# Kernel optimization log

Measured on AMD Instinct MI355X. Metric: run time of the kernel, lower is better.

Reference implementation:

```python
import jax, jax.numpy as jnp
import numpy as np
import math

B, S, D_IN, D_Q = 4, 2048, 512, 512

def setup_inputs() -> dict:
    key = jax.random.key(0)
    ks = jax.random.split(key, 7)
    s_in = 1.0 / math.sqrt(D_IN)
    x = jax.random.normal(ks[0], (B, S, D_IN), dtype=jnp.float32)
    # nn.Linear-style params: W [out,in], b [out]; uniform(-1/sqrt(in), 1/sqrt(in))
    Wq = jax.random.uniform(ks[1], (D_Q, D_IN), jnp.float32, -s_in, s_in)
    bq = jax.random.uniform(ks[2], (D_Q,), jnp.float32, -s_in, s_in)
    Wk = jax.random.uniform(ks[3], (D_Q, D_IN), jnp.float32, -s_in, s_in)
    bk = jax.random.uniform(ks[4], (D_Q,), jnp.float32, -s_in, s_in)
    Wv = jax.random.uniform(ks[5], (D_Q, D_IN), jnp.float32, -s_in, s_in)
    bv = jax.random.uniform(ks[6], (D_Q,), jnp.float32, -s_in, s_in)
    return {"x": x, "Wq": Wq, "bq": bq, "Wk": Wk, "bk": bk, "Wv": Wv, "bv": bv}

def reference(x, Wq, bq, Wk, bk, Wv, bv):
    # Q/K/V projections: [B,S,D_IN] @ W^T + b -> [B,S,D_Q]
    Q = jnp.einsum('bsi,qi->bsq', x, Wq) + bq
    K = jnp.einsum('bsi,qi->bsq', x, Wk) + bk
    V = jnp.einsum('bsi,qi->bsq', x, Wv) + bv
    scale = 1.0 / math.sqrt(D_Q)
    scores = jnp.einsum('bsq,btq->bst', Q, K) * scale  # [B,S,S]
    attention = jax.nn.softmax(scores, axis=-1)        # 'atten_prob'
    weighted = jnp.einsum('bst,btq->bsq', attention, V)  # 'atten_score'
    return (attention, weighted)
```

## Files before the change

kernel.cpp:

```cpp
#include <hip/hip_runtime.h>
#include <hip/hip_bf16.h>

typedef unsigned short u16;
typedef short bf16x8 __attribute__((ext_vector_type(8)));
typedef float f32x4 __attribute__((ext_vector_type(4)));

#define S_LEN 2048
#define DQ 512
#define NBATCH 4

__device__ __forceinline__ u16 f2bf(float f) {
    __hip_bfloat16 h = __float2bfloat16(f);
    return *reinterpret_cast<u16*>(&h);
}
__device__ __forceinline__ float bf2f(u16 u) {
    unsigned v = ((unsigned)u) << 16;
    union { unsigned u; float f; } c; c.u = v; return c.f;
}

__device__ __forceinline__ void async16(const u16* g, u16* l) {
    __builtin_amdgcn_global_load_lds(
        (__attribute__((address_space(1))) void*)g,
        (__attribute__((address_space(3))) void*)l, 16, 0, 0);
}

__device__ __forceinline__ int xcd_swz(int bid, int chunk) {
    return (bid & 7) * chunk + (bid >> 3);
}

__global__ __launch_bounds__(256) void k_cvt_all(const float* __restrict__ x,
                                                 const float* __restrict__ wq,
                                                 const float* __restrict__ wk,
                                                 const float* __restrict__ wv,
                                                 u16* __restrict__ xb, u16* __restrict__ wb,
                                                 float* __restrict__ sums) {
    int bid = blockIdx.x;
    if (bid >= 4864) {
        int i = (bid - 4864) * 256 + threadIdx.x;
        *(f32x4*)(sums + (size_t)i * 4) = (f32x4)0.0f;
        return;
    }
    const float* src;
    u16* dst;
    int i;
    if (bid < 4096)      { src = x;  dst = xb;          i = bid * 256 + threadIdx.x; }
    else if (bid < 4352) { src = wq; dst = wb;          i = (bid - 4096) * 256 + threadIdx.x; }
    else if (bid < 4608) { src = wk; dst = wb + 262144; i = (bid - 4352) * 256 + threadIdx.x; }
    else                 { src = wv; dst = wb + 524288; i = (bid - 4608) * 256 + threadIdx.x; }
    f32x4 v = *(const f32x4*)(src + (size_t)i * 4);
    ushort4 o;
    o.x = f2bf(v.x); o.y = f2bf(v.y); o.z = f2bf(v.z); o.w = f2bf(v.w);
    *(ushort4*)(dst + (size_t)i * 4) = o;
}

__device__ __forceinline__ void stage_unit(const u16* __restrict__ G, u16* buf,
                                           int kcol, int h, int tid) {
#pragma unroll
    for (int q = 0; q < 2; ++q) {
        int c   = q * 512 + tid;
        int r   = c >> 3;
        int p   = c & 7;
        int lch = p ^ (r & 7);
        async16(G + (size_t)(h * 128 + r) * DQ + kcol + lch * 8,
                buf + h * 8192 + c * 8);
    }
}

__device__ __forceinline__ void gemm256(const u16* __restrict__ A, const u16* __restrict__ B,
                                        u16* ldsA, u16* ldsB, f32x4 acc[8][4], int tid) {
    const int lane = tid & 63;
    const int w    = tid >> 6;
    const int wr   = w >> 2;
    const int wc   = w & 3;
    const int l16  = lane & 15;
    const int quad = lane >> 4;
    const int p0   = quad ^ (l16 & 7);
    const int a0   = (wr * 128 + l16) * 64 + p0 * 8;
    const int a1   = (wr * 128 + l16) * 64 + (p0 ^ 4) * 8;
    const int b0   = (wc * 64 + l16) * 64 + p0 * 8;
    const int b1   = (wc * 64 + l16) * 64 + (p0 ^ 4) * 8;

    stage_unit(A, ldsA, 0, 0, tid);
    stage_unit(A, ldsA, 0, 1, tid);
    stage_unit(B, ldsB, 0, 0, tid);
    stage_unit(B, ldsB, 0, 1, tid);
    __syncthreads();

    for (int kt = 0; kt < 8; ++kt) {
        const u16* rdA = ldsA + (kt & 1) * 16384;
        const u16* rdB = ldsB + (kt & 1) * 16384;
        u16* wrA = ldsA + ((kt + 1) & 1) * 16384;
        u16* wrB = ldsB + ((kt + 1) & 1) * 16384;
        const int  kc = (kt + 1) * 64;
        const bool pf = kt < 7;
        bf16x8 a[4][2], bbf[2][2];

        if (pf) { stage_unit(A, wrA, kc, 0, tid); stage_unit(A, wrA, kc, 1, tid); }
#pragma unroll
        for (int i = 0; i < 4; ++i) {
            a[i][0] = *(const bf16x8*)(rdA + a0 + i * 1024);
            a[i][1] = *(const bf16x8*)(rdA + a1 + i * 1024);
        }
#pragma unroll
        for (int j = 0; j < 2; ++j) {
            bbf[j][0] = *(const bf16x8*)(rdB + b0 + j * 1024);
            bbf[j][1] = *(const bf16x8*)(rdB + b1 + j * 1024);
        }
        __builtin_amdgcn_s_setprio(1);
#pragma unroll
        for (int i = 0; i < 4; ++i)
#pragma unroll
            for (int j = 0; j < 2; ++j) {
                acc[i][j] = __builtin_amdgcn_mfma_f32_16x16x32_bf16(a[i][0], bbf[j][0], acc[i][j], 0, 0, 0);
                acc[i][j] = __builtin_amdgcn_mfma_f32_16x16x32_bf16(a[i][1], bbf[j][1], acc[i][j], 0, 0, 0);
            }
        __builtin_amdgcn_s_setprio(0);

        if (pf) { stage_unit(B, wrB, kc, 0, tid); stage_unit(B, wrB, kc, 1, tid); }
#pragma unroll
        for (int j = 0; j < 2; ++j) {
            bbf[j][0] = *(const bf16x8*)(rdB + b0 + (2 + j) * 1024);
            bbf[j][1] = *(const bf16x8*)(rdB + b1 + (2 + j) * 1024);
        }
        __builtin_amdgcn_s_setprio(1);
#pragma unroll
        for (int i = 0; i < 4; ++i)
#pragma unroll
            for (int j = 0; j < 2; ++j) {
                acc[i][2 + j] = __builtin_amdgcn_mfma_f32_16x16x32_bf16(a[i][0], bbf[j][0], acc[i][2 + j], 0, 0, 0);
                acc[i][2 + j] = __builtin_amdgcn_mfma_f32_16x16x32_bf16(a[i][1], bbf[j][1], acc[i][2 + j], 0, 0, 0);
            }
        __builtin_amdgcn_s_setprio(0);

#pragma unroll
        for (int i = 0; i < 4; ++i) {
            a[i][0] = *(const bf16x8*)(rdA + a0 + (4 + i) * 1024);
            a[i][1] = *(const bf16x8*)(rdA + a1 + (4 + i) * 1024);
        }
        __builtin_amdgcn_s_setprio(1);
#pragma unroll
        for (int i = 0; i < 4; ++i)
#pragma unroll
            for (int j = 0; j < 2; ++j) {
                acc[4 + i][2 + j] = __builtin_amdgcn_mfma_f32_16x16x32_bf16(a[i][0], bbf[j][0], acc[4 + i][2 + j], 0, 0, 0);
                acc[4 + i][2 + j] = __builtin_amdgcn_mfma_f32_16x16x32_bf16(a[i][1], bbf[j][1], acc[4 + i][2 + j], 0, 0, 0);
            }
        __builtin_amdgcn_s_setprio(0);

#pragma unroll
        for (int j = 0; j < 2; ++j) {
            bbf[j][0] = *(const bf16x8*)(rdB + b0 + j * 1024);
            bbf[j][1] = *(const bf16x8*)(rdB + b1 + j * 1024);
        }
        __builtin_amdgcn_s_setprio(1);
#pragma unroll
        for (int i = 0; i < 4; ++i)
#pragma unroll
            for (int j = 0; j < 2; ++j) {
                acc[4 + i][j] = __builtin_amdgcn_mfma_f32_16x16x32_bf16(a[i][0], bbf[j][0], acc[4 + i][j], 0, 0, 0);
                acc[4 + i][j] = __builtin_amdgcn_mfma_f32_16x16x32_bf16(a[i][1], bbf[j][1], acc[4 + i][j], 0, 0, 0);
            }
        __builtin_amdgcn_s_setprio(0);

        __syncthreads();
    }
}

__global__ __launch_bounds__(512, 2) void k_proj(const u16* __restrict__ xb, const u16* __restrict__ Wb,
                                                 const float* __restrict__ bq, const float* __restrict__ bk,
                                                 const float* __restrict__ bv, u16* __restrict__ out,
                                                 u16* __restrict__ VT) {
    __shared__ __align__(16) u16 lds[65536];
    const int l  = xcd_swz(blockIdx.x, 24);
    const int bx = l & 1;
    const int by = (l >> 1) & 31;
    const int z  = l >> 6;
    const int m0 = by * 256, n0 = bx * 256;
    const u16* A = xb + (size_t)m0 * DQ;
    const u16* B = Wb + (size_t)z * DQ * DQ + (size_t)n0 * DQ;
    const float* bias = (z == 0) ? bq : (z == 1) ? bk : bv;

    f32x4 acc[8][4];
#pragma unroll
    for (int i = 0; i < 8; ++i)
#pragma unroll
        for (int j = 0; j < 4; ++j) acc[i][j] = (f32x4)0.0f;

    const int tid = threadIdx.x;
    gemm256(A, B, lds, lds + 32768, acc, tid);

    const int lane = tid & 63, w = tid >> 6;
    const int wr = w >> 2, wc = w & 3;
    const int l16 = lane & 15, quad = lane >> 4;

    if (z < 2) {
        u16* outz = out + (size_t)z * 8192 * DQ;
#pragma unroll
        for (int j = 0; j < 4; ++j) {
            int gn = n0 + wc * 64 + j * 16 + l16;
            float bv_ = bias[gn];
#pragma unroll
            for (int i = 0; i < 8; ++i)
#pragma unroll
                for (int r = 0; r < 4; ++r) {
                    int gm = m0 + wr * 128 + i * 16 + quad * 4 + r;
                    outz[(size_t)gm * DQ + gn] = f2bf(acc[i][j][r] + bv_);
                }
        }
    } else {
        const int bb_ = m0 >> 11;
        u16* VTb_ = VT + (size_t)bb_ * DQ * S_LEN;
#pragma unroll
        for (int j = 0; j < 4; ++j) {
            int gn = n0 + wc * 64 + j * 16 + l16;
            float bv_ = bias[gn];
#pragma unroll
            for (int i = 0; i < 8; ++i) {
                int t0 = (m0 & 2047) + wr * 128 + i * 16 + quad * 4;
                ushort4 o;
                o.x = f2bf(acc[i][j][0] + bv_);
                o.y = f2bf(acc[i][j][1] + bv_);
                o.z = f2bf(acc[i][j][2] + bv_);
                o.w = f2bf(acc[i][j][3] + bv_);
                *(ushort4*)(VTb_ + (size_t)gn * S_LEN + t0) = o;
            }
        }
    }
}

__global__ __launch_bounds__(512, 2) void k_scores(const u16* __restrict__ Qb, const u16* __restrict__ Kb,
                                                   u16* __restrict__ Pb, float* __restrict__ sums) {
    __shared__ __align__(16) u16 lds[65536];
    const int l  = xcd_swz(blockIdx.x, 32);
    const int bx = l & 7;
    const int by = (l >> 3) & 7;
    const int b  = l >> 6;
    const int m0 = by * 256, n0 = bx * 256;
    const u16* A = Qb + ((size_t)b * S_LEN + m0) * DQ;
    const u16* B = Kb + ((size_t)b * S_LEN + n0) * DQ;

    f32x4 acc[8][4];
#pragma unroll
    for (int i = 0; i < 8; ++i)
#pragma unroll
        for (int j = 0; j < 4; ++j) acc[i][j] = (f32x4)0.0f;

    const int tid = threadIdx.x;
    gemm256(A, B, lds, lds + 32768, acc, tid);

    const float scale = 0.044194173824159216f;
    const int lane = tid & 63, w = tid >> 6;
    const int wr = w >> 2, wc = w & 3;
    const int l16 = lane & 15, quad = lane >> 4;
    u16* prow = Pb + (size_t)(b * S_LEN + m0) * S_LEN;

    float psum[8][4];
#pragma unroll
    for (int i = 0; i < 8; ++i)
#pragma unroll
        for (int r = 0; r < 4; ++r) psum[i][r] = 0.0f;

#pragma unroll
    for (int i = 0; i < 8; ++i)
#pragma unroll
        for (int j = 0; j < 4; ++j)
#pragma unroll
            for (int r = 0; r < 4; ++r) {
                int gm = wr * 128 + i * 16 + quad * 4 + r;
                int gn = n0 + wc * 64 + j * 16 + l16;
                float e = __expf(acc[i][j][r] * scale);
                u16 pbv = f2bf(e);
                prow[(size_t)gm * S_LEN + gn] = pbv;
                psum[i][r] += bf2f(pbv);
            }

    float* sums_row = sums + b * S_LEN + m0 + wr * 128;
#pragma unroll
    for (int i = 0; i < 8; ++i)
#pragma unroll
        for (int r = 0; r < 4; ++r) {
            float v = psum[i][r];
            v += __shfl_xor(v, 1);
            v += __shfl_xor(v, 2);
            v += __shfl_xor(v, 4);
            v += __shfl_xor(v, 8);
            if (l16 == 0) atomicAdd(&sums_row[i * 16 + quad * 4 + r], v);
        }
}

__device__ __forceinline__ void stage_pv(const u16* __restrict__ G, u16* buf,
                                         int kcol, int h, int tid) {
    int c   = tid;
    int r   = c >> 3;
    int p   = c & 7;
    int lch = p ^ (r & 7);
    async16(G + (size_t)(h * 64 + r) * S_LEN + kcol + lch * 8,
            buf + h * 4096 + c * 8);
}

__global__ __launch_bounds__(512, 2) void k_pv(const u16* __restrict__ Pb, const u16* __restrict__ VT,
                                               const float* __restrict__ sums,
                                               float* __restrict__ probs,
                                               float* __restrict__ wout) {
    __shared__ __align__(16) u16 lds[49408];
    u16* ldsA = lds;
    u16* ldsB = lds + 24576;
    float* ldsInv = (float*)(lds + 49152);
    const int l  = xcd_swz(blockIdx.x, 32);
    const int bx = l & 3;
    const int by = (l >> 2) & 15;
    const int b  = l >> 6;
    const int m0 = by * 128, n0 = bx * 128;
    const u16* A = Pb + (size_t)(b * S_LEN + m0) * S_LEN;
    const u16* B = VT + (size_t)b * DQ * S_LEN + (size_t)n0 * S_LEN;
    const u16* Psl = Pb + (size_t)(b * S_LEN + m0) * S_LEN + bx * 512;
    float* Pro = probs + ((size_t)b * S_LEN + m0) * S_LEN + bx * 512;

    const int tid  = threadIdx.x;
    const int lane = tid & 63;
    const int w    = tid >> 6;
    const int wr   = w >> 2;
    const int wc   = w & 3;
    const int l16  = lane & 15;
    const int quad = lane >> 4;
    const int p0   = quad ^ (l16 & 7);
    const int a0   = (wr * 64 + l16) * 64 + p0 * 8;
    const int a1   = (wr * 64 + l16) * 64 + (p0 ^ 4) * 8;
    const int b0   = (wc * 32 + l16) * 64 + p0 * 8;
    const int b1   = (wc * 32 + l16) * 64 + (p0 ^ 4) * 8;

    f32x4 acc[4][2];
#pragma unroll
    for (int i = 0; i < 4; ++i)
#pragma unroll
        for (int j = 0; j < 2; ++j) acc[i][j] = (f32x4)0.0f;

    float sv = 1.0f;
    if (tid < 128) sv = sums[b * S_LEN + m0 + tid];
    stage_pv(A, ldsA, 0, 0, tid);          stage_pv(A, ldsA, 0, 1, tid);
    stage_pv(B, ldsB, 0, 0, tid);          stage_pv(B, ldsB, 0, 1, tid);
    stage_pv(A, ldsA + 8192, 64, 0, tid);  stage_pv(A, ldsA + 8192, 64, 1, tid);
    stage_pv(B, ldsB + 8192, 64, 0, tid);  stage_pv(B, ldsB + 8192, 64, 1, tid);
    if (tid < 128) ldsInv[tid] = 1.0f / sv;
    asm volatile("s_waitcnt vmcnt(4) lgkmcnt(0)" ::: "memory");
    __builtin_amdgcn_s_barrier();
    __builtin_amdgcn_sched_barrier(0);

    int rb = 0;
    for (int kt = 0; kt < 32; ++kt) {
        const u16* rdA = ldsA + rb * 8192;
        const u16* rdB = ldsB + rb * 8192;

        const bool do_probs = (kt & 1) == 0;
        bf16x8 pvv;
        float pinv = 0.0f;
        float* pdst = nullptr;
        if (do_probs) {
            int idx = (kt >> 1) * 512 + tid;
            int r  = idx >> 6;
            int cc = (idx & 63) << 3;
            pvv  = *(const bf16x8*)(Psl + (size_t)r * S_LEN + cc);
            pinv = ldsInv[r];
            pdst = Pro + (size_t)r * S_LEN + cc;
        }

        if (kt < 30) {
            int wbi = rb >= 1 ? rb - 1 : 2;
            u16* wA = ldsA + wbi * 8192;
            u16* wB = ldsB + wbi * 8192;
            const int kc = (kt + 2) * 64;
            stage_pv(A, wA, kc, 0, tid);
            stage_pv(A, wA, kc, 1, tid);
            stage_pv(B, wB, kc, 0, tid);
            stage_pv(B, wB, kc, 1, tid);
        }

        bf16x8 a[4][2], bbf[2];
#pragma unroll
        for (int i = 0; i < 4; ++i) {
            a[i][0] = *(const bf16x8*)(rdA + a0 + i * 1024);
            a[i][1] = *(const bf16x8*)(rdA + a1 + i * 1024);
        }
        bbf[0] = *(const bf16x8*)(rdB + b0);
        bbf[1] = *(const bf16x8*)(rdB + b1);
        __builtin_amdgcn_s_setprio(1);
#pragma unroll
        for (int i = 0; i < 4; ++i) {
            acc[i][0] = __builtin_amdgcn_mfma_f32_16x16x32_bf16(a[i][0], bbf[0], acc[i][0], 0, 0, 0);
            acc[i][0] = __builtin_amdgcn_mfma_f32_16x16x32_bf16(a[i][1], bbf[1], acc[i][0], 0, 0, 0);
        }
        __builtin_amdgcn_s_setprio(0);

        bbf[0] = *(const bf16x8*)(rdB + b0 + 1024);
        bbf[1] = *(const bf16x8*)(rdB + b1 + 1024);
        __builtin_amdgcn_s_setprio(1);
#pragma unroll
        for (int i = 0; i < 4; ++i) {
            acc[i][1] = __builtin_amdgcn_mfma_f32_16x16x32_bf16(a[i][0], bbf[0], acc[i][1], 0, 0, 0);
            acc[i][1] = __builtin_amdgcn_mfma_f32_16x16x32_bf16(a[i][1], bbf[1], acc[i][1], 0, 0, 0);
        }
        __builtin_amdgcn_s_setprio(0);

        if (do_probs) {
            f32x4 o0, o1;
            o0.x = bf2f((u16)pvv[0]) * pinv;
            o0.y = bf2f((u16)pvv[1]) * pinv;
            o0.z = bf2f((u16)pvv[2]) * pinv;
            o0.w = bf2f((u16)pvv[3]) * pinv;
            o1.x = bf2f((u16)pvv[4]) * pinv;
            o1.y = bf2f((u16)pvv[5]) * pinv;
            o1.z = bf2f((u16)pvv[6]) * pinv;
            o1.w = bf2f((u16)pvv[7]) * pinv;
            *(f32x4*)(pdst) = o0;
            *(f32x4*)(pdst + 4) = o1;
        }

        if (kt < 31) {
            if (kt < 30) asm volatile("s_waitcnt vmcnt(6)" ::: "memory");
            else         asm volatile("s_waitcnt vmcnt(2)" ::: "memory");
            __builtin_amdgcn_s_barrier();
            __builtin_amdgcn_sched_barrier(0);
        }
        rb = (rb == 2) ? 0 : rb + 1;
    }

    float* outb = wout + (size_t)b * S_LEN * DQ;
#pragma unroll
    for (int i = 0; i < 4; ++i) {
#pragma unroll
        for (int r = 0; r < 4; ++r) {
            int lm = wr * 64 + i * 16 + quad * 4 + r;
            float inv = ldsInv[lm];
#pragma unroll
            for (int j = 0; j < 2; ++j) {
                int gn = n0 + wc * 32 + j * 16 + l16;
                outb[(size_t)(m0 + lm) * DQ + gn] = acc[i][j][r] * inv;
            }
        }
    }
}

extern "C" void kernel_launch(void* const* d_in, const int* in_sizes, int n_in,
                              void* d_out, int out_size, void* d_ws, size_t ws_size,
                              hipStream_t stream) {
    const float* x  = (const float*)d_in[0];
    const float* Wq = (const float*)d_in[1];
    const float* bq = (const float*)d_in[2];
    const float* Wk = (const float*)d_in[3];
    const float* bk = (const float*)d_in[4];
    const float* Wv = (const float*)d_in[5];
    const float* bv = (const float*)d_in[6];

    char* ws = (char*)d_ws;
    u16* xb  = (u16*)(ws);
    u16* Wb  = (u16*)(ws + 8388608);
    u16* Qb  = (u16*)(ws + 9961472);
    u16* Kb  = (u16*)(ws + 18350080);
    u16* VTb = (u16*)(ws + 35127296);
    u16* Pb  = (u16*)(ws + 43515904);
    float* sums = (float*)(ws + 77070336);
    float* probs = (float*)d_out;
    float* wout  = (float*)d_out + 16777216;

    k_cvt_all<<<4872, 256, 0, stream>>>(x, Wq, Wk, Wv, xb, Wb, sums);
    k_proj<<<192, 512, 0, stream>>>(xb, Wb, bq, bk, bv, Qb, VTb);
    k_scores<<<256, 512, 0, stream>>>(Qb, Kb, Pb, sums);
    k_pv<<<256, 512, 0, stream>>>(Pb, VTb, sums, probs, wout);
}
```

Measured before the change: 177.9 us.

## Switch GEMM mainloop to K=32 tiles with triple-buffered LDS pipeline

```diff
diff --git a/kernel.cpp b/kernel.cpp
--- a/kernel.cpp
+++ b/kernel.cpp
@@ -53,16 +53,16 @@
     *(ushort4*)(dst + (size_t)i * 4) = o;
 }
 
-__device__ __forceinline__ void stage_unit(const u16* __restrict__ G, u16* buf,
-                                           int kcol, int h, int tid) {
+__device__ __forceinline__ void stage32(const u16* __restrict__ G, u16* buf,
+                                        int kcol, int tid) {
 #pragma unroll
     for (int q = 0; q < 2; ++q) {
         int c   = q * 512 + tid;
-        int r   = c >> 3;
-        int p   = c & 7;
-        int lch = p ^ (r & 7);
-        async16(G + (size_t)(h * 128 + r) * DQ + kcol + lch * 8,
-                buf + h * 8192 + c * 8);
+        int r   = c >> 2;
+        int p   = c & 3;
+        int lch = p ^ (r & 3);
+        async16(G + (size_t)r * DQ + kcol + lch * 8,
+                buf + c * 8);
     }
 }
 
@@ -74,95 +74,78 @@
     const int wc   = w & 3;
     const int l16  = lane & 15;
     const int quad = lane >> 4;
-    const int p0   = quad ^ (l16 & 7);
-    const int a0   = (wr * 128 + l16) * 64 + p0 * 8;
-    const int a1   = (wr * 128 + l16) * 64 + (p0 ^ 4) * 8;
-    const int b0   = (wc * 64 + l16) * 64 + p0 * 8;
-    const int b1   = (wc * 64 + l16) * 64 + (p0 ^ 4) * 8;
-
-    stage_unit(A, ldsA, 0, 0, tid);
-    stage_unit(A, ldsA, 0, 1, tid);
-    stage_unit(B, ldsB, 0, 0, tid);
-    stage_unit(B, ldsB, 0, 1, tid);
-    __syncthreads();
-
-    for (int kt = 0; kt < 8; ++kt) {
-        const u16* rdA = ldsA + (kt & 1) * 16384;
-        const u16* rdB = ldsB + (kt & 1) * 16384;
-        u16* wrA = ldsA + ((kt + 1) & 1) * 16384;
-        u16* wrB = ldsB + ((kt + 1) & 1) * 16384;
-        const int  kc = (kt + 1) * 64;
-        const bool pf = kt < 7;
-        bf16x8 a[4][2], bbf[2][2];
-
-        if (pf) { stage_unit(A, wrA, kc, 0, tid); stage_unit(A, wrA, kc, 1, tid); }
-#pragma unroll
-        for (int i = 0; i < 4; ++i) {
-            a[i][0] = *(const bf16x8*)(rdA + a0 + i * 1024);
-            a[i][1] = *(const bf16x8*)(rdA + a1 + i * 1024);
-        }
-#pragma unroll
-        for (int j = 0; j < 2; ++j) {
-            bbf[j][0] = *(const bf16x8*)(rdB + b0 + j * 1024);
-            bbf[j][1] = *(const bf16x8*)(rdB + b1 + j * 1024);
-        }
+    const int pch  = (quad ^ (l16 & 3)) * 8;
+    const int a0   = (wr * 128 + l16) * 32 + pch;
+    const int b0   = (wc * 64 + l16) * 32 + pch;
+
+    stage32(A, ldsA, 0, tid);
+    stage32(B, ldsB, 0, tid);
+    stage32(A, ldsA + 8192, 32, tid);
+    stage32(B, ldsB + 8192, 32, tid);
+    asm volatile("s_waitcnt vmcnt(4)" ::: "memory");
+    __builtin_amdgcn_s_barrier();
+    __builtin_amdgcn_sched_barrier(0);
+
+    int rb = 0;
+    for (int kt = 0; kt < 16; ++kt) {
+        const u16* rdA = ldsA + rb * 8192;
+        const u16* rdB = ldsB + rb * 8192;
+
+        if (kt < 14) {
+            int wbi = rb >= 1 ? rb - 1 : 2;
+            const int kc = (kt + 2) * 32;
+            stage32(A, ldsA + wbi * 8192, kc, tid);
+            stage32(B, ldsB + wbi * 8192, kc, tid);
+        }
+
+        bf16x8 af[4], bf[4];
+#pragma unroll
+        for (int i = 0; i < 4; ++i) af[i] = *(const bf16x8*)(rdA + a0 + i * 512);
+#pragma unroll
+        for (int j = 0; j < 2; ++j) bf[j] = *(const bf16x8*)(rdB + b0 + j * 512);
         __builtin_amdgcn_s_setprio(1);
 #pragma unroll
         for (int i = 0; i < 4; ++i)
 #pragma unroll
-            for (int j = 0; j < 2; ++j) {
-                acc[i][j] = __builtin_amdgcn_mfma_f32_16x16x32_bf16(a[i][0], bbf[j][0], acc[i][j], 0, 0, 0);
-                acc[i][j] = __builtin_amdgcn_mfma_f32_16x16x32_bf16(a[i][1], bbf[j][1], acc[i][j], 0, 0, 0);
-            }
-        __builtin_amdgcn_s_setprio(0);
-
-        if (pf) { stage_unit(B, wrB, kc, 0, tid); stage_unit(B, wrB, kc, 1, tid); }
-#pragma unroll
-        for (int j = 0; j < 2; ++j) {
-            bbf[j][0] = *(const bf16x8*)(rdB + b0 + (2 + j) * 1024);
-            bbf[j][1] = *(const bf16x8*)(rdB + b1 + (2 + j) * 1024);
-        }
+            for (int j = 0; j < 2; ++j)
+                acc[i][j] = __builtin_amdgcn_mfma_f32_16x16x32_bf16(af[i], bf[j], acc[i][j], 0, 0, 0);
+        __builtin_amdgcn_s_setprio(0);
+
+#pragma unroll
+        for (int j = 0; j < 2; ++j) bf[2 + j] = *(const bf16x8*)(rdB + b0 + (2 + j) * 512);
         __builtin_amdgcn_s_setprio(1);
 #pragma unroll
         for (int i = 0; i < 4; ++i)
 #pragma unroll
-            for (int j = 0; j < 2; ++j) {
-                acc[i][2 + j] = __builtin_amdgcn_mfma_f32_16x16x32_bf16(a[i][0], bbf[j][0], acc[i][2 + j], 0, 0, 0);
-                acc[i][2 + j] = __builtin_amdgcn_mfma_f32_16x16x32_bf16(a[i][1], bbf[j][1], acc[i][2 + j], 0, 0, 0);
-            }
-        __builtin_amdgcn_s_setprio(0);
-
-#pragma unroll
-        for (int i = 0; i < 4; ++i) {
-            a[i][0] = *(const bf16x8*)(rdA + a0 + (4 + i) * 1024);
-            a[i][1] = *(const bf16x8*)(rdA + a1 + (4 + i) * 1024);
-        }
+            for (int j = 0; j < 2; ++j)
+                acc[i][2 + j] = __builtin_amdgcn_mfma_f32_16x16x32_bf16(af[i], bf[2 + j], acc[i][2 + j], 0, 0, 0);
+        __builtin_amdgcn_s_setprio(0);
+
+#pragma unroll
+        for (int i = 0; i < 4; ++i) af[i] = *(const bf16x8*)(rdA + a0 + (4 + i) * 512);
         __builtin_amdgcn_s_setprio(1);
 #pragma unroll
         for (int i = 0; i < 4; ++i)
 #pragma unroll
-            for (int j = 0; j < 2; ++j) {
-                acc[4 + i][2 + j] = __builtin_amdgcn_mfma_f32_16x16x32_bf16(a[i][0], bbf[j][0], acc[4 + i][2 + j], 0, 0, 0);
-                acc[4 + i][2 + j] = __builtin_amdgcn_mfma_f32_16x16x32_bf16(a[i][1], bbf[j][1], acc[4 + i][2 + j], 0, 0, 0);
-            }
-        __builtin_amdgcn_s_setprio(0);
-
-#pragma unroll
-        for (int j = 0; j < 2; ++j) {
-            bbf[j][0] = *(const bf16x8*)(rdB + b0 + j * 1024);
-            bbf[j][1] = *(const bf16x8*)(rdB + b1 + j * 1024);
-        }
+            for (int j = 0; j < 2; ++j)
+                acc[4 + i][2 + j] = __builtin_amdgcn_mfma_f32_16x16x32_bf16(af[i], bf[2 + j], acc[4 + i][2 + j], 0, 0, 0);
+        __builtin_amdgcn_s_setprio(0);
+
         __builtin_amdgcn_s_setprio(1);
 #pragma unroll
         for (int i = 0; i < 4; ++i)
 #pragma unroll
-            for (int j = 0; j < 2; ++j) {
-                acc[4 + i][j] = __builtin_amdgcn_mfma_f32_16x16x32_bf16(a[i][0], bbf[j][0], acc[4 + i][j], 0, 0, 0);
-                acc[4 + i][j] = __builtin_amdgcn_mfma_f32_16x16x32_bf16(a[i][1], bbf[j][1], acc[4 + i][j], 0, 0, 0);
-            }
-        __builtin_amdgcn_s_setprio(0);
-
-        __syncthreads();
+            for (int j = 0; j < 2; ++j)
+                acc[4 + i][j] = __builtin_amdgcn_mfma_f32_16x16x32_bf16(af[i], bf[j], acc[4 + i][j], 0, 0, 0);
+        __builtin_amdgcn_s_setprio(0);
+
+        if (kt < 15) {
+            if (kt < 14) asm volatile("s_waitcnt vmcnt(4)" ::: "memory");
+            else         asm volatile("s_waitcnt vmcnt(0)" ::: "memory");
+            __builtin_amdgcn_s_barrier();
+            __builtin_amdgcn_sched_barrier(0);
+        }
+        rb = (rb == 2) ? 0 : rb + 1;
     }
 }
 
@@ -170,7 +153,7 @@
                                                  const float* __restrict__ bq, const float* __restrict__ bk,
                                                  const float* __restrict__ bv, u16* __restrict__ out,
                                                  u16* __restrict__ VT) {
-    __shared__ __align__(16) u16 lds[65536];
+    __shared__ __align__(16) u16 lds[49152];
     const int l  = xcd_swz(blockIdx.x, 24);
     const int bx = l & 1;
     const int by = (l >> 1) & 31;
@@ -187,7 +170,7 @@
         for (int j = 0; j < 4; ++j) acc[i][j] = (f32x4)0.0f;
 
     const int tid = threadIdx.x;
-    gemm256(A, B, lds, lds + 32768, acc, tid);
+    gemm256(A, B, lds, lds + 24576, acc, tid);
 
     const int lane = tid & 63, w = tid >> 6;
     const int wr = w >> 2, wc = w & 3;
@@ -230,7 +213,7 @@
 
 __global__ __launch_bounds__(512, 2) void k_scores(const u16* __restrict__ Qb, const u16* __restrict__ Kb,
                                                    u16* __restrict__ Pb, float* __restrict__ sums) {
-    __shared__ __align__(16) u16 lds[65536];
+    __shared__ __align__(16) u16 lds[49152];
     const int l  = xcd_swz(blockIdx.x, 32);
     const int bx = l & 7;
     const int by = (l >> 3) & 7;
@@ -246,7 +229,7 @@
         for (int j = 0; j < 4; ++j) acc[i][j] = (f32x4)0.0f;
 
     const int tid = threadIdx.x;
-    gemm256(A, B, lds, lds + 32768, acc, tid);
+    gemm256(A, B, lds, lds + 24576, acc, tid);
 
     const float scale = 0.044194173824159216f;
     const int lane = tid & 63, w = tid >> 6;
```

Measured after the change: 182.0 us. 2.3% more time.
